# Performance work log

Measured on AMD Instinct MI355X. Metric: run time of the kernel, lower is better.

The kernel has to match this reference:

```python
import jax, jax.numpy as jnp
import numpy as np

# ---- architecture constants (match init_kwargs) ----
T, B, NA, OUT = 10, 32, 512, 128          # n_tiles, batch, atoms per sample, output_dim
HID, LMAX = 64, 3                          # hidden_dim, hidden_lmax
IN_MULS = [32, 16, 16, 16]                 # input multiplicity per l (32x0e+16x1o+16x2e+16x3o)
HID_MULS = [HID] * (LMAX + 1)              # gate_irreps multiplicities (64 per l)
DIMS = [2 * l + 1 for l in range(LMAX + 1)]
D_IN = sum(m * d for m, d in zip(IN_MULS, DIMS))   # 272
L0_OUT = HID * (LMAX + 1)                  # 256: scalars(64) + gates(192) in linear_irreps l=0 block


def setup_inputs() -> dict:
    key = jax.random.key(0)
    ks = jax.random.split(key, 12)
    inp = {
        "atom_features": jax.random.normal(ks[0], (B, NA, D_IN), jnp.float32),
        "W0_0": jax.random.normal(ks[1], (T, IN_MULS[0], L0_OUT), jnp.float32),
        "W0_1": jax.random.normal(ks[2], (T, IN_MULS[1], HID), jnp.float32),
        "W0_2": jax.random.normal(ks[3], (T, IN_MULS[2], HID), jnp.float32),
        "W0_3": jax.random.normal(ks[4], (T, IN_MULS[3], HID), jnp.float32),
        "W1_0": jax.random.normal(ks[5], (T, HID, L0_OUT), jnp.float32),
        "W1_1": jax.random.normal(ks[6], (T, HID, HID), jnp.float32),
        "W1_2": jax.random.normal(ks[7], (T, HID, HID), jnp.float32),
        "W1_3": jax.random.normal(ks[8], (T, HID, HID), jnp.float32),
        "Wout": jax.random.normal(ks[9], (T, HID, OUT), jnp.float32),
        "mlp_mapping": jax.random.randint(ks[10], (B, NA, 1), 0, 11),  # 10 == ghost
    }
    return inp


def _split(x, muls):
    """Split flat irreps feature (N, D) into per-l blocks (N, mul_l, 2l+1)."""
    blocks, off = [], 0
    for l, m in enumerate(muls):
        d = 2 * l + 1
        blocks.append(x[:, off:off + m * d].reshape(-1, m, d))
        off += m * d
    return blocks


def _linear(blocks, Ws):
    """e3nn block-diagonal Linear: mix multiplicities per l, 1/sqrt(fan_in) norm."""
    return [jnp.einsum('nmi,mo->noi', b, w) * (1.0 / np.sqrt(b.shape[1]))
            for b, w in zip(blocks, Ws)]


def _gate(blocks):
    """e3nn Gate: SiLU on scalars, SiLU(gates) multiplies each gated l>0 irrep."""
    y0 = blocks[0][..., 0]                      # (N, 256)
    scalars = jax.nn.silu(y0[:, :HID])          # (N, 64)
    gates = jax.nn.silu(y0[:, HID:])            # (N, 192) -> one gate set per l=1..3
    out = [scalars[:, :, None]]
    for l in range(1, LMAX + 1):
        g = gates[:, (l - 1) * HID: l * HID]    # (N, 64)
        out.append(blocks[l] * g[:, :, None])
    return out


def _class_mlp(x, W0s, W1s, Wout_i):
    """Per-class EquivariantMLP (dropout = identity in eval mode)."""
    b = _split(x, IN_MULS)
    b = _gate(_linear(b, W0s))                  # layer 1: Linear -> Gate
    b = _gate(_linear(b, W1s))                  # layer 2: Linear -> Gate
    s = b[0][..., 0]                            # scalar (0e) channels (N, 64)
    return (s @ Wout_i) * (1.0 / np.sqrt(HID))  # readout to OUT scalars


def reference(atom_features, W0_0, W0_1, W0_2, W0_3, W1_0, W1_1, W1_2, W1_3, Wout, mlp_mapping):
    mapping = mlp_mapping[..., 0]               # (B, NA)
    x = atom_features.reshape(B * NA, D_IN)
    outs = []
    for i in range(T):                          # small fixed expert loop
        W0s = [W0_0[i], W0_1[i], W0_2[i], W0_3[i]]
        W1s = [W1_0[i], W1_1[i], W1_2[i], W1_3[i]]
        y = _class_mlp(x, W0s, W1s, Wout[i]).reshape(B, NA, OUT)
        mask = (mapping == i).astype(y.dtype)   # class-i dispatch (ghost id 10 never matches)
        outs.append(jnp.sum(y * mask[..., None], axis=1))  # scatter-sum per batch row
    return jnp.concatenate(outs, axis=1)        # (B, T*OUT)
```

## Files before the change

### kernel.cpp

```cpp
#include <hip/hip_runtime.h>


#define NCLS  10
#define NB    32
#define NATOM 512
#define DIN   272

__global__ __launch_bounds__(256) void eqmlp_fused(
    const float* __restrict__ x,
    const float* __restrict__ W0,
    const float* __restrict__ W1,
    const float* __restrict__ Wo,
    const int*   __restrict__ mapping,
    float*       __restrict__ out)
{
    const int c    = blockIdx.x;
    const int b    = blockIdx.y;
    const int tid  = threadIdx.x;
    const int w    = tid >> 6;
    const int lane = tid & 63;

    __shared__ __align__(16) float W0s[32 * 64];
    __shared__ __align__(16) float W1s[64 * 64];
    __shared__ __align__(16) float Wos[64 * 128];
    __shared__ __align__(16) float xbuf [4][32 * 4];
    __shared__ __align__(16) float h1buf[4][64 * 4];
    __shared__ __align__(16) float hsbuf[4][64];
    __shared__ __align__(16) float red[4 * 128];

    {
        const float4* g0 = (const float4*)(W0 + (size_t)c * 32 * 256);
        float4* s = (float4*)W0s;
        for (int i = tid; i < 32 * 64 / 4; i += 256)
            s[i] = g0[(i >> 4) * 64 + (i & 15)];
        const float4* g1 = (const float4*)(W1 + (size_t)c * 64 * 256);
        float4* s1 = (float4*)W1s;
        for (int i = tid; i < 64 * 64 / 4; i += 256)
            s1[i] = g1[(i >> 4) * 64 + (i & 15)];
        const float4* g2 = (const float4*)(Wo + (size_t)c * 64 * 128);
        float4* s2 = (float4*)Wos;
        for (int i = tid; i < 64 * 128 / 4; i += 256)
            s2[i] = g2[i];
    }
    __syncthreads();

    float accA = 0.f, accB = 0.f;

    const int*   map_b = mapping + b * NATOM;
    const float* x_b   = x + (size_t)b * NATOM * DIN;
    const float  sc0   = 0.17677669529663689f;
    const float  sc1   = 0.125f;

    for (int chunk = 0; chunk < 2; ++chunk) {
        const int base = w * 128 + chunk * 64;
        const int mv   = map_b[base + lane];
        unsigned long long mask = __ballot(mv == c);

        while (mask) {
            int a0 = 0, a1 = 0, a2 = 0, a3 = 0, na = 0;
            {             int p = __builtin_ctzll(mask); mask &= mask - 1; a0 = base + p; na = 1; }
            if (mask)   { int p = __builtin_ctzll(mask); mask &= mask - 1; a1 = base + p; na = 2; }
            if (mask)   { int p = __builtin_ctzll(mask); mask &= mask - 1; a2 = base + p; na = 3; }
            if (mask)   { int p = __builtin_ctzll(mask); mask &= mask - 1; a3 = base + p; na = 4; }

            {
                const int m  = lane & 31;
                const int jh = lane >> 5;
                const int e0 = jh ? a1 : a0;
                const int e1 = jh ? a3 : a2;
                float v0 = (jh     < na) ? x_b[(size_t)e0 * DIN + m] : 0.f;
                float v1 = (jh + 2 < na) ? x_b[(size_t)e1 * DIN + m] : 0.f;
                xbuf[w][m * 4 + jh]     = v0;
                xbuf[w][m * 4 + jh + 2] = v1;
            }
            __builtin_amdgcn_wave_barrier();

            float h0 = 0.f, h1 = 0.f, h2 = 0.f, h3 = 0.f;
            #pragma unroll
            for (int m = 0; m < 32; ++m) {
                float  wv = W0s[m * 64 + lane];
                float4 xv = *(const float4*)&xbuf[w][m * 4];
                h0 += xv.x * wv; h1 += xv.y * wv; h2 += xv.z * wv; h3 += xv.w * wv;
            }
            h0 *= sc0; h1 *= sc0; h2 *= sc0; h3 *= sc0;
            h0 = h0 / (1.f + __expf(-h0));
            h1 = h1 / (1.f + __expf(-h1));
            h2 = h2 / (1.f + __expf(-h2));
            h3 = h3 / (1.f + __expf(-h3));
            *(float4*)&h1buf[w][lane * 4] = make_float4(h0, h1, h2, h3);
            __builtin_amdgcn_wave_barrier();

            float z0 = 0.f, z1 = 0.f, z2 = 0.f, z3 = 0.f;
            #pragma unroll
            for (int m = 0; m < 64; ++m) {
                float  wv = W1s[m * 64 + lane];
                float4 hv = *(const float4*)&h1buf[w][m * 4];
                z0 += hv.x * wv; z1 += hv.y * wv; z2 += hv.z * wv; z3 += hv.w * wv;
            }
            z0 *= sc1; z1 *= sc1; z2 *= sc1; z3 *= sc1;
            z0 = z0 / (1.f + __expf(-z0));
            z1 = z1 / (1.f + __expf(-z1));
            z2 = z2 / (1.f + __expf(-z2));
            z3 = z3 / (1.f + __expf(-z3));
            hsbuf[w][lane] = z0 + z1 + z2 + z3;
            __builtin_amdgcn_wave_barrier();

            #pragma unroll
            for (int m = 0; m < 64; m += 4) {
                float4 hv = *(const float4*)&hsbuf[w][m];
                accA += hv.x * Wos[(m + 0) * 128 + lane];
                accB += hv.x * Wos[(m + 0) * 128 + 64 + lane];
                accA += hv.y * Wos[(m + 1) * 128 + lane];
                accB += hv.y * Wos[(m + 1) * 128 + 64 + lane];
                accA += hv.z * Wos[(m + 2) * 128 + lane];
                accB += hv.z * Wos[(m + 2) * 128 + 64 + lane];
                accA += hv.w * Wos[(m + 3) * 128 + lane];
                accB += hv.w * Wos[(m + 3) * 128 + 64 + lane];
            }
        }
    }

    red[w * 128 + lane]      = accA;
    red[w * 128 + 64 + lane] = accB;
    __syncthreads();
    if (tid < 128) {
        float s = red[tid] + red[128 + tid] + red[256 + tid] + red[384 + tid];
        out[(size_t)b * (NCLS * 128) + c * 128 + tid] = s * 0.125f;
    }
}

extern "C" void kernel_launch(void* const* d_in, const int* in_sizes, int n_in,
                              void* d_out, int out_size, void* d_ws, size_t ws_size,
                              hipStream_t stream) {
    const float* x  = (const float*)d_in[0];
    const float* W0 = (const float*)d_in[1];
    const float* W1 = (const float*)d_in[5];
    const float* Wo = (const float*)d_in[9];
    const int*   mp = (const int*)  d_in[10];
    float* outp = (float*)d_out;

    dim3 grid(NCLS, NB);
    eqmlp_fused<<<grid, 256, 0, stream>>>(x, W0, W1, Wo, mp, outp);
}
```

Before: 105.3 us.

## Sum gated scalars before readout and apply output matmul once per block

Because the readout is linear, the gated scalar outputs are summed over all atoms of the class first, and the Wout matmul runs once per block instead of once per atom group. The Wout shared-memory staging (32KB) is removed and its weights are read straight from global memory in the small final GEMV. Mapping loads are also hoisted ahead of the weight staging. This cuts per-atom work and shared memory use, which should raise occupancy, but it changes the floating-point summation order.

Result: faster. 98.87 us (-6.1%).

```diff
diff --git a/kernel.cpp b/kernel.cpp
--- a/kernel.cpp
+++ b/kernel.cpp
@@ -22,39 +22,36 @@
 
     __shared__ __align__(16) float W0s[32 * 64];
     __shared__ __align__(16) float W1s[64 * 64];
-    __shared__ __align__(16) float Wos[64 * 128];
     __shared__ __align__(16) float xbuf [4][32 * 4];
     __shared__ __align__(16) float h1buf[4][64 * 4];
-    __shared__ __align__(16) float hsbuf[4][64];
-    __shared__ __align__(16) float red[4 * 128];
+    __shared__ __align__(16) float hsum[4][64];
+    __shared__ __align__(16) float fin[2][128];
+
+    const int* map_b = mapping + b * NATOM;
+    const int  mv0 = map_b[w * 128 + lane];
+    const int  mv1 = map_b[w * 128 + 64 + lane];
 
     {
         const float4* g0 = (const float4*)(W0 + (size_t)c * 32 * 256);
-        float4* s = (float4*)W0s;
+        float4* s0 = (float4*)W0s;
         for (int i = tid; i < 32 * 64 / 4; i += 256)
-            s[i] = g0[(i >> 4) * 64 + (i & 15)];
+            s0[i] = g0[(i >> 4) * 64 + (i & 15)];
         const float4* g1 = (const float4*)(W1 + (size_t)c * 64 * 256);
         float4* s1 = (float4*)W1s;
         for (int i = tid; i < 64 * 64 / 4; i += 256)
             s1[i] = g1[(i >> 4) * 64 + (i & 15)];
-        const float4* g2 = (const float4*)(Wo + (size_t)c * 64 * 128);
-        float4* s2 = (float4*)Wos;
-        for (int i = tid; i < 64 * 128 / 4; i += 256)
-            s2[i] = g2[i];
     }
     __syncthreads();
 
-    float accA = 0.f, accB = 0.f;
+    float zacc = 0.f;
 
-    const int*   map_b = mapping + b * NATOM;
-    const float* x_b   = x + (size_t)b * NATOM * DIN;
-    const float  sc0   = 0.17677669529663689f;
-    const float  sc1   = 0.125f;
+    const float* x_b = x + (size_t)b * NATOM * DIN;
+    const float  sc0 = 0.17677669529663689f;
+    const float  sc1 = 0.125f;
 
     for (int chunk = 0; chunk < 2; ++chunk) {
         const int base = w * 128 + chunk * 64;
-        const int mv   = map_b[base + lane];
-        unsigned long long mask = __ballot(mv == c);
+        unsigned long long mask = __ballot((chunk ? mv1 : mv0) == c);
 
         while (mask) {
             int a0 = 0, a1 = 0, a2 = 0, a3 = 0, na = 0;
@@ -98,35 +95,38 @@
                 z0 += hv.x * wv; z1 += hv.y * wv; z2 += hv.z * wv; z3 += hv.w * wv;
             }
             z0 *= sc1; z1 *= sc1; z2 *= sc1; z3 *= sc1;
-            z0 = z0 / (1.f + __expf(-z0));
-            z1 = z1 / (1.f + __expf(-z1));
-            z2 = z2 / (1.f + __expf(-z2));
-            z3 = z3 / (1.f + __expf(-z3));
-            hsbuf[w][lane] = z0 + z1 + z2 + z3;
+            zacc += z0 / (1.f + __expf(-z0));
+            zacc += z1 / (1.f + __expf(-z1));
+            zacc += z2 / (1.f + __expf(-z2));
+            zacc += z3 / (1.f + __expf(-z3));
             __builtin_amdgcn_wave_barrier();
-
-            #pragma unroll
-            for (int m = 0; m < 64; m += 4) {
-                float4 hv = *(const float4*)&hsbuf[w][m];
-                accA += hv.x * Wos[(m + 0) * 128 + lane];
-                accB += hv.x * Wos[(m + 0) * 128 + 64 + lane];
-                accA += hv.y * Wos[(m + 1) * 128 + lane];
-                accB += hv.y * Wos[(m + 1) * 128 + 64 + lane];
-                accA += hv.z * Wos[(m + 2) * 128 + lane];
-                accB += hv.z * Wos[(m + 2) * 128 + 64 + lane];
-                accA += hv.w * Wos[(m + 3) * 128 + lane];
-                accB += hv.w * Wos[(m + 3) * 128 + 64 + lane];
-            }
         }
     }
 
-    red[w * 128 + lane]      = accA;
-    red[w * 128 + 64 + lane] = accB;
+    hsum[w][lane] = zacc;
     __syncthreads();
-    if (tid < 128) {
-        float s = red[tid] + red[128 + tid] + red[256 + tid] + red[384 + tid];
-        out[(size_t)b * (NCLS * 128) + c * 128 + tid] = s * 0.125f;
+    if (tid < 64)
+        hsum[0][tid] += hsum[1][tid] + hsum[2][tid] + hsum[3][tid];
+    __syncthreads();
+
+    const int col  = tid & 127;
+    const int half = tid >> 7;
+    const float* Wo_c = Wo + (size_t)c * 64 * 128 + col;
+    float acc = 0.f;
+    #pragma unroll
+    for (int mm = 0; mm < 32; mm += 4) {
+        const int m = half * 32 + mm;
+        float4 hv = *(const float4*)&hsum[0][m];
+        acc += hv.x * Wo_c[(size_t)(m + 0) * 128];
+        acc += hv.y * Wo_c[(size_t)(m + 1) * 128];
+        acc += hv.z * Wo_c[(size_t)(m + 2) * 128];
+        acc += hv.w * Wo_c[(size_t)(m + 3) * 128];
     }
+    fin[half][col] = acc;
+    __syncthreads();
+    if (tid < 128)
+        out[(size_t)b * (NCLS * 128) + c * 128 + tid]
+            = (fin[0][tid] + fin[1][tid]) * 0.125f;
 }
 
 extern "C" void kernel_launch(void* const* d_in, const int* in_sizes, int n_in,
```
